# Optimization experiments

Hardware: AMD Instinct MI355X
Metric: run time of the kernel (lower is better)

## Reference

```python
import jax, jax.numpy as jnp
import numpy as np

NUM_FEATURES = 20480
NUM_ACC = 128
BATCH = 4096
SPARSITY_P = 0.0015  # ~30 active features per position, like real NNUE


def setup_inputs() -> dict:
    key = jax.random.key(0)
    kw, kb, k1, k2, k3, k4 = jax.random.split(key, 6)
    # sparse binary one-hot-per-piece feature vectors
    white = (jax.random.uniform(kw, (BATCH, NUM_FEATURES)) < SPARSITY_P).astype(jnp.float32)
    black = (jax.random.uniform(kb, (BATCH, NUM_FEATURES)) < SPARSITY_P).astype(jnp.float32)
    psqt_w = jax.random.normal(k1, (2, NUM_FEATURES), dtype=jnp.float32) * 0.02
    acc_w = jax.random.normal(k2, (NUM_ACC, NUM_FEATURES), dtype=jnp.float32) * 0.02
    acc_b = jax.random.normal(k3, (NUM_ACC,), dtype=jnp.float32) * 0.02
    out_w = jax.random.normal(k4, (2, NUM_ACC), dtype=jnp.float32) * 0.1
    return {"white": white, "black": black, "psqt_w": psqt_w,
            "acc_w": acc_w, "acc_b": acc_b, "out_w": out_w}


def _side(x, psqt_w, acc_w, acc_b, out_w):
    # psqt: [B,2]; accumulator: [B,128]; CReLU then Linear(128->2, no bias)
    psqt = x @ psqt_w.T                              # [B, 2]
    acc = jnp.clip(x @ acc_w.T + acc_b, 0.0, 1.0)    # [B, 128]
    pos = acc @ out_w.T                              # [B, 2]
    return psqt, pos


def reference(white, black, psqt_w, acc_w, acc_b, out_w):
    psqt_w_, pos_w = _side(white, psqt_w, acc_w, acc_b, out_w)
    psqt_b, pos_b = _side(black, psqt_w, acc_w, acc_b, out_w)
    return (psqt_w_ - psqt_b) + (pos_w - pos_b)      # [B, 2]
```

## Files before the change

### kernel.cpp

```cpp
#include <hip/hip_runtime.h>

#define NF     20480
#define NACC   128
#define BATCH  4096
#define MAXI_W 64

typedef unsigned int uvec4 __attribute__((ext_vector_type(4)));

__device__ __forceinline__ float bflo(unsigned int w) {
    union { unsigned int u; float f; } v; v.u = w << 16; return v.f;
}
__device__ __forceinline__ float bfhi(unsigned int w) {
    union { unsigned int u; float f; } v; v.u = w & 0xFFFF0000u; return v.f;
}
__device__ __forceinline__ unsigned short f2bf(float f) {
    union { float f; unsigned int i; } v; v.f = f;
    unsigned int x = v.i;
    return (unsigned short)((x + 0x7FFFu + ((x >> 16) & 1u)) >> 16);
}

__global__ __launch_bounds__(256) void transpose_accw(const float* __restrict__ acc_w,
                                                      unsigned short* __restrict__ accT) {
    __shared__ float tile[NACC][33];
    const int t  = threadIdx.x;
    const int f0 = blockIdx.x * 32;
    const int fl = t & 31;
    const int cr = t >> 5;
    #pragma unroll
    for (int i = 0; i < 16; ++i) {
        int cc = i * 8 + cr;
        tile[cc][fl] = acc_w[(size_t)cc * NF + f0 + fl];
    }
    __syncthreads();
    const int c2 = t & 63;
    const int fr = t >> 6;
    #pragma unroll
    for (int i = 0; i < 8; ++i) {
        int ff = i * 4 + fr;
        unsigned int u = ((unsigned int)f2bf(tile[c2 * 2 + 1][ff]) << 16)
                       |  (unsigned int)f2bf(tile[c2 * 2][ff]);
        *(unsigned int*)(accT + (size_t)(f0 + ff) * NACC + c2 * 2) = u;
    }
}

#define BALLOT_COMPACT(d, fidx)                                             \
    {                                                                       \
        unsigned long long m = __ballot((d) != 0u);                         \
        if (m) {                                                            \
            unsigned int pre = __builtin_amdgcn_mbcnt_lo((unsigned int)m, 0u); \
            pre = __builtin_amdgcn_mbcnt_hi((unsigned int)(m >> 32), pre);  \
            int slot = base + (int)pre;                                     \
            if ((d) != 0u && slot < MAXI_W) idx[slot] = (fidx);             \
            base += (int)__popcll(m);                                       \
        }                                                                   \
    }

#define PROCQ(c, fb0)                                                       \
    {                                                                       \
        unsigned int any = (c).x | (c).y | (c).z | (c).w;                   \
        if (__ballot(any != 0u)) {                                          \
            BALLOT_COMPACT((c).x, (fb0) + 0)                                \
            BALLOT_COMPACT((c).y, (fb0) + 1)                                \
            BALLOT_COMPACT((c).z, (fb0) + 2)                                \
            BALLOT_COMPACT((c).w, (fb0) + 3)                                \
        }                                                                   \
    }

#define PROC16(c0, c1, c2, c3, fb)                                         \
    PROCQ(c0, (fb))        PROCQ(c1, (fb) + 512)                           \
    PROCQ(c2, (fb) + 1024) PROCQ(c3, (fb) + 1536)

__global__ __launch_bounds__(256) void nnue_main(
    const float* __restrict__ white,
    const float* __restrict__ black,
    const float* __restrict__ psqt_w,
    const unsigned short* __restrict__ accT,
    const float* __restrict__ acc_b,
    const float* __restrict__ out_w,
    float* __restrict__ out)
{
    __shared__ int   s_cnt[2][2];
    __shared__ int   s_idx[2][2][MAXI_W];
    __shared__ float s_part[2][2][NACC];
    __shared__ float s_red[8];

    const int t    = threadIdx.x;
    const int b    = blockIdx.x;
    const int side = t >> 7;
    const int wv   = (t >> 6) & 1;
    const int lt   = t & 127;
    const int lane = t & 63;

    const float bias = acc_b[lt];
    const float ow0  = out_w[lt];
    const float ow1  = out_w[NACC + lt];
    const float sgn  = side ? -1.f : 1.f;

    const float* X  = (side ? black : white) + (size_t)b * NF;
    const uvec4* Xv = (const uvec4*)X;

    int* idx = s_idx[side][wv];
    int  base = 0;

    uvec4 c0 = __builtin_nontemporal_load(&Xv[lt]);
    uvec4 c1 = __builtin_nontemporal_load(&Xv[lt + 128]);
    uvec4 c2 = __builtin_nontemporal_load(&Xv[lt + 256]);
    uvec4 c3 = __builtin_nontemporal_load(&Xv[lt + 384]);

    #pragma unroll 1
    for (int i = 0; i < 10; ++i) {
        uvec4 n0 = {0,0,0,0}, n1 = {0,0,0,0}, n2 = {0,0,0,0}, n3 = {0,0,0,0};
        if (i < 9) {
            const int v = (i + 1) * 512 + lt;
            n0 = __builtin_nontemporal_load(&Xv[v]);
            n1 = __builtin_nontemporal_load(&Xv[v + 128]);
            n2 = __builtin_nontemporal_load(&Xv[v + 256]);
            n3 = __builtin_nontemporal_load(&Xv[v + 384]);
        }
        const int fb = (i * 512 + lt) * 4;
        PROC16(c0, c1, c2, c3, fb)
        c0 = n0; c1 = n1; c2 = n2; c3 = n3;
    }
    if (lane == 0) s_cnt[side][wv] = base;
    __syncthreads();

    const int n0c = min(s_cnt[side][0], MAXI_W);
    const int n1c = min(s_cnt[side][1], MAXI_W);
    const int n   = n0c + n1c;

    float ps0 = 0.f, ps1 = 0.f;
    if (lt < n) {
        int f = (lt < n0c) ? s_idx[side][0][lt] : s_idx[side][1][lt - n0c];
        ps0 = psqt_w[f];
        ps1 = psqt_w[NF + f];
    }

    const int  nw  = wv ? n1c : n0c;
    const int* seg = s_idx[side][wv];
    float a0 = 0.f, a1 = 0.f;
    #pragma unroll 4
    for (int j = 0; j < nw; ++j) {
        int f = seg[j];
        unsigned int w = *(const unsigned int*)(accT + (size_t)f * NACC + lane * 2);
        a0 += bflo(w); a1 += bfhi(w);
    }
    s_part[side][wv][lane * 2]     = a0;
    s_part[side][wv][lane * 2 + 1] = a1;
    __syncthreads();

    float a  = s_part[side][0][lt] + s_part[side][1][lt];
    float h  = fminf(fmaxf(a + bias, 0.f), 1.f);
    float p0 = sgn * (h * ow0 + ps0);
    float p1 = sgn * (h * ow1 + ps1);

    #pragma unroll
    for (int off = 32; off > 0; off >>= 1) {
        p0 += __shfl_down(p0, off, 64);
        p1 += __shfl_down(p1, off, 64);
    }
    if ((t & 63) == 0) { int w8 = t >> 6; s_red[w8 * 2] = p0; s_red[w8 * 2 + 1] = p1; }
    __syncthreads();

    if (t == 0) {
        out[(size_t)b * 2 + 0] = s_red[0] + s_red[2] + s_red[4] + s_red[6];
        out[(size_t)b * 2 + 1] = s_red[1] + s_red[3] + s_red[5] + s_red[7];
    }
}

extern "C" void kernel_launch(void* const* d_in, const int* in_sizes, int n_in,
                              void* d_out, int out_size, void* d_ws, size_t ws_size,
                              hipStream_t stream) {
    const float* white  = (const float*)d_in[0];
    const float* black  = (const float*)d_in[1];
    const float* psqt_w = (const float*)d_in[2];
    const float* acc_w  = (const float*)d_in[3];
    const float* acc_b  = (const float*)d_in[4];
    const float* out_w  = (const float*)d_in[5];
    float* out = (float*)d_out;

    unsigned short* accT = (unsigned short*)d_ws;

    transpose_accw<<<NF / 32, 256, 0, stream>>>(acc_w, accT);
    nnue_main<<<BATCH, 256, 0, stream>>>(white, black, psqt_w, accT,
                                         acc_b, out_w, out);
}
```

Measured before the change: 606.1 us.

## Split NNUE into scan and accumulate kernels with atomic global index lists

Splits the fused kernel into a scan kernel and an accumulate kernel. The scan kernel collects the active feature indices into per-position global lists using global atomics, replacing the wave ballot compaction. The accumulate kernel reads those lists and sums the transposed bf16 weight rows, with the two waves interleaving over the same list. The change also drops the nontemporal loads and zeroes the counters inside the transpose kernel. In exchange it adds a third launch, a round trip for the index lists through global memory, and atomic traffic on one counter per position, which makes the index order nondeterministic.

```diff
diff --git a/kernel.cpp b/kernel.cpp
--- a/kernel.cpp
+++ b/kernel.cpp
@@ -3,7 +3,7 @@
 #define NF     20480
 #define NACC   128
 #define BATCH  4096
-#define MAXI_W 64
+#define MAXI   96
 
 typedef unsigned int uvec4 __attribute__((ext_vector_type(4)));
 
@@ -20,7 +20,10 @@
 }
 
 __global__ __launch_bounds__(256) void transpose_accw(const float* __restrict__ acc_w,
-                                                      unsigned short* __restrict__ accT) {
+                                                      unsigned short* __restrict__ accT,
+                                                      int* __restrict__ cnt) {
+    if (blockIdx.x < 32) cnt[blockIdx.x * 256 + threadIdx.x] = 0;
+
     __shared__ float tile[NACC][33];
     const int t  = threadIdx.x;
     const int f0 = blockIdx.x * 32;
@@ -43,44 +46,71 @@
     }
 }
 
-#define BALLOT_COMPACT(d, fidx)                                             \
-    {                                                                       \
-        unsigned long long m = __ballot((d) != 0u);                         \
-        if (m) {                                                            \
-            unsigned int pre = __builtin_amdgcn_mbcnt_lo((unsigned int)m, 0u); \
-            pre = __builtin_amdgcn_mbcnt_hi((unsigned int)(m >> 32), pre);  \
-            int slot = base + (int)pre;                                     \
-            if ((d) != 0u && slot < MAXI_W) idx[slot] = (fidx);             \
-            base += (int)__popcll(m);                                       \
-        }                                                                   \
+#define EMIT(d, f)                                                        \
+    if ((d) != 0u) {                                                      \
+        int p = atomicAdd(mycnt, 1);                                      \
+        if (p < MAXI) myidx[p] = (f);                                     \
     }
 
-#define PROCQ(c, fb0)                                                       \
-    {                                                                       \
-        unsigned int any = (c).x | (c).y | (c).z | (c).w;                   \
-        if (__ballot(any != 0u)) {                                          \
-            BALLOT_COMPACT((c).x, (fb0) + 0)                                \
-            BALLOT_COMPACT((c).y, (fb0) + 1)                                \
-            BALLOT_COMPACT((c).z, (fb0) + 2)                                \
-            BALLOT_COMPACT((c).w, (fb0) + 3)                                \
-        }                                                                   \
+#define PROCQ(c, f0)                                                      \
+    if (((c).x | (c).y | (c).z | (c).w) != 0u) {                          \
+        EMIT((c).x, (f0) + 0)                                             \
+        EMIT((c).y, (f0) + 1)                                             \
+        EMIT((c).z, (f0) + 2)                                             \
+        EMIT((c).w, (f0) + 3)                                             \
     }
 
-#define PROC16(c0, c1, c2, c3, fb)                                         \
-    PROCQ(c0, (fb))        PROCQ(c1, (fb) + 512)                           \
-    PROCQ(c2, (fb) + 1024) PROCQ(c3, (fb) + 1536)
-
-__global__ __launch_bounds__(256) void nnue_main(
+__global__ __launch_bounds__(256) void nnue_scan(
     const float* __restrict__ white,
     const float* __restrict__ black,
+    int* __restrict__ cnt,
+    int* __restrict__ gidx)
+{
+    const int t    = threadIdx.x;
+    const int b    = blockIdx.x;
+    const int side = t >> 7;
+    const int lt   = t & 127;
+
+    const float* X  = (side ? black : white) + (size_t)b * NF;
+    const uvec4* Xv = (const uvec4*)X;
+
+    int* mycnt = cnt + side * BATCH + b;
+    int* myidx = gidx + ((size_t)side * BATCH + b) * MAXI;
+
+    uvec4 c0 = Xv[lt];
+    uvec4 c1 = Xv[lt + 128];
+    uvec4 c2 = Xv[lt + 256];
+    uvec4 c3 = Xv[lt + 384];
+
+    #pragma unroll 1
+    for (int i = 0; i < 10; ++i) {
+        uvec4 n0 = {0,0,0,0}, n1 = {0,0,0,0}, n2 = {0,0,0,0}, n3 = {0,0,0,0};
+        if (i < 9) {
+            const int v = (i + 1) * 512 + lt;
+            n0 = Xv[v];
+            n1 = Xv[v + 128];
+            n2 = Xv[v + 256];
+            n3 = Xv[v + 384];
+        }
+        const int fb = (i * 512 + lt) * 4;
+        PROCQ(c0, fb)
+        PROCQ(c1, fb + 512)
+        PROCQ(c2, fb + 1024)
+        PROCQ(c3, fb + 1536)
+        c0 = n0; c1 = n1; c2 = n2; c3 = n3;
+    }
+}
+
+__global__ __launch_bounds__(256) void nnue_out(
     const float* __restrict__ psqt_w,
     const unsigned short* __restrict__ accT,
     const float* __restrict__ acc_b,
     const float* __restrict__ out_w,
+    const int* __restrict__ cnt,
+    const int* __restrict__ gidx,
     float* __restrict__ out)
 {
-    __shared__ int   s_cnt[2][2];
-    __shared__ int   s_idx[2][2][MAXI_W];
+    __shared__ int   s_list[2][MAXI];
     __shared__ float s_part[2][2][NACC];
     __shared__ float s_red[8];
 
@@ -91,62 +121,33 @@
     const int lt   = t & 127;
     const int lane = t & 63;
 
-    const float bias = acc_b[lt];
-    const float ow0  = out_w[lt];
-    const float ow1  = out_w[NACC + lt];
-    const float sgn  = side ? -1.f : 1.f;
-
-    const float* X  = (side ? black : white) + (size_t)b * NF;
-    const uvec4* Xv = (const uvec4*)X;
-
-    int* idx = s_idx[side][wv];
-    int  base = 0;
-
-    uvec4 c0 = __builtin_nontemporal_load(&Xv[lt]);
-    uvec4 c1 = __builtin_nontemporal_load(&Xv[lt + 128]);
-    uvec4 c2 = __builtin_nontemporal_load(&Xv[lt + 256]);
-    uvec4 c3 = __builtin_nontemporal_load(&Xv[lt + 384]);
-
-    #pragma unroll 1
-    for (int i = 0; i < 10; ++i) {
-        uvec4 n0 = {0,0,0,0}, n1 = {0,0,0,0}, n2 = {0,0,0,0}, n3 = {0,0,0,0};
-        if (i < 9) {
-            const int v = (i + 1) * 512 + lt;
-            n0 = __builtin_nontemporal_load(&Xv[v]);
-            n1 = __builtin_nontemporal_load(&Xv[v + 128]);
-            n2 = __builtin_nontemporal_load(&Xv[v + 256]);
-            n3 = __builtin_nontemporal_load(&Xv[v + 384]);
-        }
-        const int fb = (i * 512 + lt) * 4;
-        PROC16(c0, c1, c2, c3, fb)
-        c0 = n0; c1 = n1; c2 = n2; c3 = n3;
-    }
-    if (lane == 0) s_cnt[side][wv] = base;
+    const int n = min(cnt[side * BATCH + b], MAXI);
+    const int* myidx = gidx + ((size_t)side * BATCH + b) * MAXI;
+    if (lt < n) s_list[side][lt] = myidx[lt];
     __syncthreads();
-
-    const int n0c = min(s_cnt[side][0], MAXI_W);
-    const int n1c = min(s_cnt[side][1], MAXI_W);
-    const int n   = n0c + n1c;
 
     float ps0 = 0.f, ps1 = 0.f;
     if (lt < n) {
-        int f = (lt < n0c) ? s_idx[side][0][lt] : s_idx[side][1][lt - n0c];
+        int f = s_list[side][lt];
         ps0 = psqt_w[f];
         ps1 = psqt_w[NF + f];
     }
 
-    const int  nw  = wv ? n1c : n0c;
-    const int* seg = s_idx[side][wv];
     float a0 = 0.f, a1 = 0.f;
-    #pragma unroll 4
-    for (int j = 0; j < nw; ++j) {
-        int f = seg[j];
+    #pragma unroll 2
+    for (int j = wv; j < n; j += 2) {
+        int f = s_list[side][j];
         unsigned int w = *(const unsigned int*)(accT + (size_t)f * NACC + lane * 2);
         a0 += bflo(w); a1 += bfhi(w);
     }
     s_part[side][wv][lane * 2]     = a0;
     s_part[side][wv][lane * 2 + 1] = a1;
     __syncthreads();
+
+    const float bias = acc_b[lt];
+    const float ow0  = out_w[lt];
+    const float ow1  = out_w[NACC + lt];
+    const float sgn  = side ? -1.f : 1.f;
 
     float a  = s_part[side][0][lt] + s_part[side][1][lt];
     float h  = fminf(fmaxf(a + bias, 0.f), 1.f);
@@ -179,8 +180,11 @@
     float* out = (float*)d_out;
 
     unsigned short* accT = (unsigned short*)d_ws;
+    int* cnt  = (int*)((char*)d_ws + 5242880);
+    int* gidx = (int*)((char*)d_ws + 5242880 + 32768);
 
-    transpose_accw<<<NF / 32, 256, 0, stream>>>(acc_w, accT);
-    nnue_main<<<BATCH, 256, 0, stream>>>(white, black, psqt_w, accT,
-                                         acc_b, out_w, out);
+    transpose_accw<<<NF / 32, 256, 0, stream>>>(acc_w, accT, cnt);
+    nnue_scan<<<BATCH, 256, 0, stream>>>(white, black, cnt, gidx);
+    nnue_out<<<BATCH, 256, 0, stream>>>(psqt_w, accT, acc_b, out_w,
+                                        cnt, gidx, out);
 }
```

New measurement: 662.0 us. +9.2%, slower.
